# Optimization experiments

Hardware: AMD Instinct MI355X
Metric: run time of the kernel (lower is better)

Reference implementation:

```python
import jax, jax.numpy as jnp
import numpy as np

DIM = 128
NUM_HEADS = 8


def setup_inputs() -> dict:
    key = jax.random.key(0)
    ks = jax.random.split(key, 5)
    B, L, C = 4, 16384, DIM
    x = jax.random.normal(ks[0], (B, L, C), dtype=jnp.float32)
    # Linear params (stored as (in, out) so y = x @ W + b)
    w_qkv = jax.random.normal(ks[1], (C, 3 * C), dtype=jnp.float32) * (C ** -0.5)
    b_qkv = jax.random.normal(ks[2], (3 * C,), dtype=jnp.float32) * 0.02
    w_proj = jax.random.normal(ks[3], (C, C), dtype=jnp.float32) * (C ** -0.5)
    b_proj = jax.random.normal(ks[4], (C,), dtype=jnp.float32) * 0.02
    return {"x": x, "w_qkv": w_qkv, "b_qkv": b_qkv, "w_proj": w_proj, "b_proj": b_proj}


def reference(x, w_qkv, b_qkv, w_proj, b_proj):
    B, L, C = x.shape
    H = NUM_HEADS
    hd = C // H
    scale = C ** -0.5  # note: torch code scales by dim**-0.5, not head_dim**-0.5

    qkv = x @ w_qkv + b_qkv                      # (B, L, 3C)
    q, k, v = jnp.split(qkv, 3, axis=-1)         # each (B, L, C)

    def to_heads(t):
        return t.reshape(B, L, H, hd).transpose(0, 2, 1, 3)  # (B, H, L, hd)

    q, k, v = to_heads(q), to_heads(k), to_heads(v)

    # Per-token outer product over head_dim: (B, H, L, hd, hd)
    attn = (q * scale)[..., :, None] * k[..., None, :]
    attn = jax.nn.softmax(attn, axis=-1)

    # attn @ v per token: (B, H, L, hd)
    out = jnp.einsum("bhlij,bhlj->bhli", attn, v)
    out = out.transpose(0, 2, 1, 3).reshape(B, L, C)  # (B, L, C)
    return out @ w_proj + b_proj
```

## Files before the change

### kernel.cpp

```cpp
#include <hip/hip_runtime.h>


typedef __attribute__((ext_vector_type(8))) short bf16x8;
typedef __attribute__((ext_vector_type(4))) float f32x4;
typedef __attribute__((ext_vector_type(4))) unsigned int u32x4;

#define TILE_M 32
#define HALF_M 16
#define QKV_STRIDE_F 388
#define O_STRIDE 136

__device__ __forceinline__ unsigned short f2bf(float f) {
    unsigned int u = __builtin_bit_cast(unsigned int, f);
    u += 0x8000u;
    return (unsigned short)(u >> 16);
}
__device__ __forceinline__ unsigned int pkbf(float lo, float hi) {
    unsigned int a = __builtin_bit_cast(unsigned int, lo) + 0x8000u;
    unsigned int b = __builtin_bit_cast(unsigned int, hi) + 0x8000u;
    return __builtin_amdgcn_perm(b, a, 0x07060302u);
}

__global__ void prep_weights(const float* __restrict__ wqkv,
                             const float* __restrict__ wproj,
                             unsigned short* __restrict__ wqkvT,
                             unsigned short* __restrict__ wprojT) {
    int idx = blockIdx.x * 256 + threadIdx.x;
    if (idx < 384 * 128) {
        int n = idx >> 7, k = idx & 127;
        wqkvT[idx] = f2bf(wqkv[k * 384 + n]);
    }
    if (idx < 128 * 128) {
        int n = idx >> 7, k = idx & 127;
        wprojT[idx] = f2bf(wproj[k * 128 + n]);
    }
}

__global__ __launch_bounds__(256, 4) void fused_channel_attn(
    const float* __restrict__ x,
    const unsigned short* __restrict__ wqkvT,
    const float* __restrict__ bqkv,
    const unsigned short* __restrict__ wprojT,
    const float* __restrict__ bproj,
    float* __restrict__ out)
{
    __shared__ __align__(16) float us_f[HALF_M * QKV_STRIDE_F];
    __shared__ __align__(16) unsigned short us_o[HALF_M * O_STRIDE];

    const int tid  = threadIdx.x;
    const int lane = tid & 63;
    const int wave = tid >> 6;
    const int col  = lane & 15;
    const int quad = lane >> 4;
    const long base_tok = (long)blockIdx.x * TILE_M;

    const int nb = wave * 6;

    bf16x8 afr[2][4];
#pragma unroll
    for (int m = 0; m < 2; ++m) {
        const float* xrow = x + (base_tok + m * 16 + col) * 128;
#pragma unroll
        for (int ks = 0; ks < 4; ++ks) {
            const float4* p = (const float4*)(xrow + ks * 32 + quad * 8);
            float4 f0 = p[0], f1 = p[1];
            u32x4 a = {pkbf(f0.x, f0.y), pkbf(f0.z, f0.w),
                       pkbf(f1.x, f1.y), pkbf(f1.z, f1.w)};
            afr[m][ks] = __builtin_bit_cast(bf16x8, a);
        }
    }

    f32x4 acc[2][6];
#pragma unroll
    for (int j = 0; j < 6; ++j) {
        float b = bqkv[(nb + j) * 16 + col];
        acc[0][j] = (f32x4){b, b, b, b};
        acc[1][j] = (f32x4){b, b, b, b};
    }
#pragma unroll
    for (int ks = 0; ks < 4; ++ks) {
        bf16x8 bfr[6];
#pragma unroll
        for (int j = 0; j < 6; ++j)
            bfr[j] = *(const bf16x8*)&wqkvT[((nb + j) * 16 + col) * 128 + ks * 32 + quad * 8];
#pragma unroll
        for (int j = 0; j < 6; ++j) {
            acc[0][j] = __builtin_amdgcn_mfma_f32_16x16x32_bf16(afr[0][ks], bfr[j], acc[0][j], 0, 0, 0);
            acc[1][j] = __builtin_amdgcn_mfma_f32_16x16x32_bf16(afr[1][ks], bfr[j], acc[1][j], 0, 0, 0);
        }
    }

    const int t  = tid & 15;
    const int h  = (tid >> 4) & 7;
    const int ih = tid >> 7;
    const float sl2e = 0.08838834764831845f * 1.44269504088896340f;

    auto write_qkv_half = [&](int m) {
#pragma unroll
        for (int j = 0; j < 6; ++j)
#pragma unroll
            for (int r = 0; r < 4; ++r)
                us_f[(quad * 4 + r) * QKV_STRIDE_F + (nb + j) * 16 + col] = acc[m][j][r];
    };

    auto stage_b_half = [&]() {
        const float* qkvrow = us_f + t * QKV_STRIDE_F + h * 16;
        float4 qv4[2], kv4[4], vv4[4];
        qv4[0] = ((const float4*)(qkvrow + ih * 8))[0];
        qv4[1] = ((const float4*)(qkvrow + ih * 8))[1];
#pragma unroll
        for (int c = 0; c < 4; ++c) {
            kv4[c] = ((const float4*)(qkvrow + 128))[c];
            vv4[c] = ((const float4*)(qkvrow + 256))[c];
        }
        float qv[8], kf[16], vf[16];
#pragma unroll
        for (int c = 0; c < 2; ++c) {
            qv[4*c] = qv4[c].x; qv[4*c+1] = qv4[c].y; qv[4*c+2] = qv4[c].z; qv[4*c+3] = qv4[c].w;
        }
#pragma unroll
        for (int c = 0; c < 4; ++c) {
            kf[4*c] = kv4[c].x; kf[4*c+1] = kv4[c].y; kf[4*c+2] = kv4[c].z; kf[4*c+3] = kv4[c].w;
            vf[4*c] = vv4[c].x; vf[4*c+1] = vv4[c].y; vf[4*c+2] = vv4[c].z; vf[4*c+3] = vv4[c].w;
        }
        float ov[8];
#pragma unroll
        for (int i = 0; i < 8; ++i) {
            float qs = qv[i] * sl2e;
            float den = 0.f, num = 0.f;
#pragma unroll
            for (int j = 0; j < 16; ++j) {
                float e = __builtin_amdgcn_exp2f(qs * kf[j]);
                den += e;
                num = fmaf(e, vf[j], num);
            }
            ov[i] = num * __builtin_amdgcn_rcpf(den);
        }
        u32x4 o0 = {pkbf(ov[0], ov[1]), pkbf(ov[2], ov[3]),
                    pkbf(ov[4], ov[5]), pkbf(ov[6], ov[7])};
        *(u32x4*)&us_o[t * O_STRIDE + h * 16 + ih * 8] = o0;
    };

    auto stage_c_half = [&](int m) {
        const int nb2 = wave * 2;
        bf16x8 af[4];
#pragma unroll
        for (int ks = 0; ks < 4; ++ks)
            af[ks] = *(const bf16x8*)&us_o[col * O_STRIDE + ks * 32 + quad * 8];
        f32x4 acc2[2];
#pragma unroll
        for (int n = 0; n < 2; ++n) {
            float b = bproj[(nb2 + n) * 16 + col];
            acc2[n] = (f32x4){b, b, b, b};
        }
#pragma unroll
        for (int ks = 0; ks < 4; ++ks) {
            bf16x8 bb[2];
#pragma unroll
            for (int n = 0; n < 2; ++n)
                bb[n] = *(const bf16x8*)&wprojT[((nb2 + n) * 16 + col) * 128 + ks * 32 + quad * 8];
#pragma unroll
            for (int n = 0; n < 2; ++n)
                acc2[n] = __builtin_amdgcn_mfma_f32_16x16x32_bf16(af[ks], bb[n], acc2[n], 0, 0, 0);
        }
#pragma unroll
        for (int n = 0; n < 2; ++n)
#pragma unroll
            for (int r = 0; r < 4; ++r) {
                long tt = base_tok + m * 16 + quad * 4 + r;
                out[tt * 128 + (nb2 + n) * 16 + col] = acc2[n][r];
            }
    };

    write_qkv_half(0);
    __syncthreads();
    stage_b_half();
    __syncthreads();
    write_qkv_half(1);
    stage_c_half(0);
    __syncthreads();
    stage_b_half();
    __syncthreads();
    stage_c_half(1);
}

extern "C" void kernel_launch(void* const* d_in, const int* in_sizes, int n_in,
                              void* d_out, int out_size, void* d_ws, size_t ws_size,
                              hipStream_t stream) {
    const float* x     = (const float*)d_in[0];
    const float* wqkv  = (const float*)d_in[1];
    const float* bqkv  = (const float*)d_in[2];
    const float* wproj = (const float*)d_in[3];
    const float* bproj = (const float*)d_in[4];
    float* out = (float*)d_out;

    unsigned short* wqkvT  = (unsigned short*)d_ws;
    unsigned short* wprojT = wqkvT + 384 * 128;

    prep_weights<<<192, 256, 0, stream>>>(wqkv, wproj, wqkvT, wprojT);

    const int tokens = in_sizes[0] / 128;
    fused_channel_attn<<<tokens / TILE_M, 256, 0, stream>>>(
        x, wqkvT, bqkv, wprojT, bproj, out);
}
```

Before: 138.7 us.

## Remap QKV tiles so each wave owns its heads, dropping block barriers

Reassigns the QKV GEMM output tiles so each wave computes the q, k and v columns of the two heads it later processes in the attention step. The attention stage then reads only LDS data written by its own wave, so the per-half block-wide __syncthreads are removed. The attention output buffer is doubled to hold both token halves, and the projection GEMM runs once after a single barrier. The cost is more shared memory for the output tile and less interleaving of the projection with attention.

After: 129.6 us. -6.5%, faster.

```diff
diff --git a/kernel.cpp b/kernel.cpp
--- a/kernel.cpp
+++ b/kernel.cpp
@@ -45,7 +45,7 @@
     float* __restrict__ out)
 {
     __shared__ __align__(16) float us_f[HALF_M * QKV_STRIDE_F];
-    __shared__ __align__(16) unsigned short us_o[HALF_M * O_STRIDE];
+    __shared__ __align__(16) unsigned short us_o[TILE_M * O_STRIDE];
 
     const int tid  = threadIdx.x;
     const int lane = tid & 63;
@@ -54,7 +54,10 @@
     const int quad = lane >> 4;
     const long base_tok = (long)blockIdx.x * TILE_M;
 
-    const int nb = wave * 6;
+    int ntile[6];
+    ntile[0] = 2 * wave;      ntile[1] = 2 * wave + 1;
+    ntile[2] = 8 + 2 * wave;  ntile[3] = 9 + 2 * wave;
+    ntile[4] = 16 + 2 * wave; ntile[5] = 17 + 2 * wave;
 
     bf16x8 afr[2][4];
 #pragma unroll
@@ -73,7 +76,7 @@
     f32x4 acc[2][6];
 #pragma unroll
     for (int j = 0; j < 6; ++j) {
-        float b = bqkv[(nb + j) * 16 + col];
+        float b = bqkv[ntile[j] * 16 + col];
         acc[0][j] = (f32x4){b, b, b, b};
         acc[1][j] = (f32x4){b, b, b, b};
     }
@@ -82,7 +85,7 @@
         bf16x8 bfr[6];
 #pragma unroll
         for (int j = 0; j < 6; ++j)
-            bfr[j] = *(const bf16x8*)&wqkvT[((nb + j) * 16 + col) * 128 + ks * 32 + quad * 8];
+            bfr[j] = *(const bf16x8*)&wqkvT[(ntile[j] * 16 + col) * 128 + ks * 32 + quad * 8];
 #pragma unroll
         for (int j = 0; j < 6; ++j) {
             acc[0][j] = __builtin_amdgcn_mfma_f32_16x16x32_bf16(afr[0][ks], bfr[j], acc[0][j], 0, 0, 0);
@@ -90,9 +93,11 @@
         }
     }
 
-    const int t  = tid & 15;
-    const int h  = (tid >> 4) & 7;
-    const int ih = tid >> 7;
+    const int t    = lane & 15;
+    const int hbit = (lane >> 4) & 1;
+    const int ih   = lane >> 5;
+    const int h    = 2 * wave + hbit;
+    const float* qkvrow = us_f + t * QKV_STRIDE_F + h * 16;
     const float sl2e = 0.08838834764831845f * 1.44269504088896340f;
 
     auto write_qkv_half = [&](int m) {
@@ -100,12 +105,11 @@
         for (int j = 0; j < 6; ++j)
 #pragma unroll
             for (int r = 0; r < 4; ++r)
-                us_f[(quad * 4 + r) * QKV_STRIDE_F + (nb + j) * 16 + col] = acc[m][j][r];
+                us_f[(quad * 4 + r) * QKV_STRIDE_F + ntile[j] * 16 + col] = acc[m][j][r];
     };
 
-    auto stage_b_half = [&]() {
-        const float* qkvrow = us_f + t * QKV_STRIDE_F + h * 16;
-        float4 qv4[2], kv4[4], vv4[4];
+    float4 qv4[2], kv4[4], vv4[4];
+    auto read_half = [&]() {
         qv4[0] = ((const float4*)(qkvrow + ih * 8))[0];
         qv4[1] = ((const float4*)(qkvrow + ih * 8))[1];
 #pragma unroll
@@ -113,6 +117,9 @@
             kv4[c] = ((const float4*)(qkvrow + 128))[c];
             vv4[c] = ((const float4*)(qkvrow + 256))[c];
         }
+    };
+
+    auto compute_attn = [&](int mhalf) {
         float qv[8], kf[16], vf[16];
 #pragma unroll
         for (int c = 0; c < 2; ++c) {
@@ -138,15 +145,25 @@
         }
         u32x4 o0 = {pkbf(ov[0], ov[1]), pkbf(ov[2], ov[3]),
                     pkbf(ov[4], ov[5]), pkbf(ov[6], ov[7])};
-        *(u32x4*)&us_o[t * O_STRIDE + h * 16 + ih * 8] = o0;
+        *(u32x4*)&us_o[(mhalf * 16 + t) * O_STRIDE + h * 16 + ih * 8] = o0;
     };
 
-    auto stage_c_half = [&](int m) {
-        const int nb2 = wave * 2;
+    write_qkv_half(0);
+    read_half();
+    write_qkv_half(1);
+    compute_attn(0);
+    read_half();
+    compute_attn(1);
+
+    __syncthreads();
+
+    const int nb2 = wave * 2;
+#pragma unroll
+    for (int m = 0; m < 2; ++m) {
         bf16x8 af[4];
 #pragma unroll
         for (int ks = 0; ks < 4; ++ks)
-            af[ks] = *(const bf16x8*)&us_o[col * O_STRIDE + ks * 32 + quad * 8];
+            af[ks] = *(const bf16x8*)&us_o[(m * 16 + col) * O_STRIDE + ks * 32 + quad * 8];
         f32x4 acc2[2];
 #pragma unroll
         for (int n = 0; n < 2; ++n) {
@@ -170,18 +187,7 @@
                 long tt = base_tok + m * 16 + quad * 4 + r;
                 out[tt * 128 + (nb2 + n) * 16 + col] = acc2[n][r];
             }
-    };
-
-    write_qkv_half(0);
-    __syncthreads();
-    stage_b_half();
-    __syncthreads();
-    write_qkv_half(1);
-    stage_c_half(0);
-    __syncthreads();
-    stage_b_half();
-    __syncthreads();
-    stage_c_half(1);
+    }
 }
 
 extern "C" void kernel_launch(void* const* d_in, const int* in_sizes, int n_in,
```
